# Kernel optimization log

Measured on AMD Instinct MI355X. Metric: run time of the kernel, lower is better.

The kernel has to match this reference:

```python
import jax, jax.numpy as jnp
import numpy as np

N, C_IN, H, W = 32, 16, 256, 256
C_OUT, K = 64, 3

def setup_inputs() -> dict:
    key = jax.random.key(0)
    kx, kw, kb = jax.random.split(key, 3)
    x = jax.random.normal(kx, (N, C_IN, H, W), dtype=jnp.float32)
    # PyTorch Conv2d default init: U(-b, b), b = 1/sqrt(fan_in)
    bound = 1.0 / np.sqrt(C_IN * K * K)
    conv_weight = jax.random.uniform(kw, (C_OUT, C_IN, K, K), minval=-bound, maxval=bound, dtype=jnp.float32)
    conv_bias = jax.random.uniform(kb, (C_OUT,), minval=-bound, maxval=bound, dtype=jnp.float32)
    return {"x": x, "conv_weight": conv_weight, "conv_bias": conv_bias}

def reference(x, conv_weight, conv_bias):
    # conv2d, stride=1, padding=0 (VALID), NCHW / OIHW
    y = jax.lax.conv_general_dilated(
        x, conv_weight,
        window_strides=(1, 1), padding="VALID",
        dimension_numbers=("NCHW", "OIHW", "NCHW"))
    y = y + conv_bias[None, :, None, None]
    # min over output channels (keepdim -> 1 channel), then double tanh
    y = jnp.min(y, axis=1, keepdims=True)  # [N,1,OH,OW]
    return jnp.tanh(jnp.tanh(y))
```

## Files before the change

kernel.cpp:

```cpp
#include <hip/hip_runtime.h>

typedef __bf16 bf16x8 __attribute__((ext_vector_type(8)));
typedef unsigned short us8 __attribute__((ext_vector_type(8)));
typedef unsigned short us2 __attribute__((ext_vector_type(2)));
typedef float f32x16 __attribute__((ext_vector_type(16)));

#define N_IMG 32
#define CI 16
#define HH 256
#define WW 256
#define CO 64
#define OHH 254
#define OWW 254

#define XS_W 258
#define SC 24
#define NSTRIP 24
#define WP_SHORTS (CO * 160)
#define WS_NEEDED ((size_t)WP_SHORTS * 2)

__device__ __forceinline__ unsigned short f2bf(float f) {
  union { float f; unsigned u; } v; v.f = f;
  return (unsigned short)((v.u + 0x7FFFu + ((v.u >> 16) & 1u)) >> 16);
}

#if defined(__has_builtin)
#if __has_builtin(__builtin_amdgcn_cvt_pk_bf16_f32)
#define HAVE_CVT_PK 1
#endif
#endif

__device__ __forceinline__ us2 cvt2(float a, float b) {
#ifdef HAVE_CVT_PK
  typedef __bf16 bf16x2 __attribute__((ext_vector_type(2)));
  bf16x2 r = __builtin_amdgcn_cvt_pk_bf16_f32(a, b);
  return __builtin_bit_cast(us2, r);
#else
  us2 r; r[0] = f2bf(a); r[1] = f2bf(b); return r;
#endif
}

__device__ __forceinline__ float fast_tanh(float x) {
  float cx = fminf(fmaxf(x, -15.f), 15.f);
  float e = __expf(2.f * cx);
  return (e - 1.f) / (e + 1.f);
}

__global__ void prep_w(const float* __restrict__ wg, const float* __restrict__ bg,
                       unsigned short* __restrict__ wp) {
  int idx = blockIdx.x * 256 + threadIdx.x;
  if (idx >= WP_SHORTS) return;
  int oc = idx / 160;
  int k = idx - oc * 160;
  int tap = k >> 4, ci = k & 15;
  float v;
  if (tap < 9)      v = wg[oc * 144 + ci * 9 + tap];
  else if (ci == 0) v = bg[oc];
  else              v = 0.f;
  wp[idx] = f2bf(v);
}

__global__ __launch_bounds__(256, 3)
void conv_fused(const float* __restrict__ xg, const unsigned short* __restrict__ wp,
                float* __restrict__ out) {
  __shared__ __align__(16) unsigned short xs[4 * XS_W * SC];
  const int t = threadIdx.x;
  const int n = blockIdx.x / NSTRIP;
  const int s = blockIdx.x - n * NSTRIP;
  const int oh0 = s * 10 + (s < 14 ? s : 14);
  const int nrows = (s < 14) ? 11 : 10;
  const int oh1 = oh0 + nrows;

  const float* srcT = xg + (size_t)n * (CI * HH * WW) + t;

  {
    float v[3][16];
#pragma unroll
    for (int r = 0; r < 3; ++r)
#pragma unroll
      for (int j = 0; j < 16; ++j)
        v[r][j] = srcT[((size_t)j * HH + (oh0 + r)) * WW];
#pragma unroll
    for (int r = 0; r < 3; ++r) {
      union { us8 v8[2]; us2 v2[8]; } pk;
#pragma unroll
      for (int j = 0; j < 8; ++j) pk.v2[j] = cvt2(v[r][2 * j], v[r][2 * j + 1]);
      const int slot = (oh0 + r) & 3;
      *(us8*)(xs + (slot * XS_W + t) * SC) = pk.v8[0];
      *(us8*)(xs + (slot * XS_W + t) * SC + 8) = pk.v8[1];
    }
  }
  if (t < 128) {
    const int slot = t >> 5, rem = t & 31;
    xs[(slot * XS_W + 256 + (rem >> 4)) * SC + (rem & 15)] = 0;
  }

  const int lane = t & 63, wave = t >> 6;
  const int lr = lane & 31, qh = lane >> 5;

  const unsigned short* wpl = wp + lr * 160 + qh * 8;
  bf16x8 afrag[2][10];
#pragma unroll
  for (int mt = 0; mt < 2; ++mt)
#pragma unroll
    for (int tap = 0; tap < 10; ++tap)
      afrag[mt][tap] =
          __builtin_bit_cast(bf16x8, *(const us8*)(wpl + mt * 32 * 160 + tap * 16));

  us8 onev = {};
  if (qh == 0) onev[0] = 0x3F80;
  const bf16x8 xone = __builtin_bit_cast(bf16x8, onev);

  const int pb = wave * 64;

  __syncthreads();

  for (int oh = oh0; oh < oh1; ++oh) {
    const bool do_stage = (oh + 1 < oh1);

    float v[16];
    if (do_stage) {
#pragma unroll
      for (int j = 0; j < 16; ++j)
        v[j] = srcT[((size_t)j * HH + (oh + 3)) * WW];
    }

    float vmin[2];
#pragma unroll
    for (int nt = 0; nt < 2; ++nt) {
      f32x16 acc0, acc1;
#pragma unroll
      for (int e = 0; e < 16; ++e) { acc0[e] = 0.f; acc1[e] = 0.f; }
#pragma unroll
      for (int tap = 0; tap < 9; ++tap) {
        const int kh = tap / 3, kw = tap - kh * 3;
        const int slot = (oh + kh) & 3;
        bf16x8 xf = __builtin_bit_cast(
            bf16x8,
            *(const us8*)(xs + (slot * XS_W + pb + nt * 32 + lr + kw) * SC + qh * 8));
        acc0 = __builtin_amdgcn_mfma_f32_32x32x16_bf16(afrag[0][tap], xf, acc0, 0, 0, 0);
        acc1 = __builtin_amdgcn_mfma_f32_32x32x16_bf16(afrag[1][tap], xf, acc1, 0, 0, 0);
      }
      acc0 = __builtin_amdgcn_mfma_f32_32x32x16_bf16(afrag[0][9], xone, acc0, 0, 0, 0);
      acc1 = __builtin_amdgcn_mfma_f32_32x32x16_bf16(afrag[1][9], xone, acc1, 0, 0, 0);

      float mv = acc0[0];
#pragma unroll
      for (int e = 1; e < 16; ++e) mv = fminf(mv, acc0[e]);
#pragma unroll
      for (int e = 0; e < 16; ++e) mv = fminf(mv, acc1[e]);
      mv = fminf(mv, __shfl_xor(mv, 32, 64));
      vmin[nt] = fast_tanh(fast_tanh(mv));
    }

    if (do_stage) {
      union { us8 v8[2]; us2 v2[8]; } pk;
#pragma unroll
      for (int j = 0; j < 8; ++j) pk.v2[j] = cvt2(v[2 * j], v[2 * j + 1]);
      const int slot = (oh + 3) & 3;
      *(us8*)(xs + (slot * XS_W + t) * SC) = pk.v8[0];
      *(us8*)(xs + (slot * XS_W + t) * SC + 8) = pk.v8[1];
    }

    const float res = (lane < 32) ? vmin[0] : vmin[1];
    const int ow = pb + lane;
    if (ow < OWW) out[((size_t)n * OHH + oh) * OWW + ow] = res;

    __syncthreads();
  }
}

#define XS_C 24
#define WS_K 168
__global__ __launch_bounds__(256, 2)
void conv_min_tanh(const float* __restrict__ xg, const float* __restrict__ wg,
                   const float* __restrict__ bg, float* __restrict__ out) {
  __shared__ __align__(16) unsigned short xs[3 * XS_W * XS_C];
  __shared__ __align__(16) unsigned short ws[CO * WS_K];
  const int t = threadIdx.x;
  const int n = blockIdx.x / OHH;
  const int oh = blockIdx.x % OHH;
#pragma unroll
  for (int i = 0; i < 36; ++i) {
    int f = i * 256 + t;
    int oc = f / 144;
    int r = f - oc * 144;
    int ci = r / 9;
    int tap = r - ci * 9;
    ws[oc * WS_K + tap * 16 + ci] = f2bf(wg[f]);
  }
  if (t < CO) ws[t * WS_K + 144] = f2bf(bg[t]);
  for (int i = t; i < CO * 15; i += 256) {
    int oc = i / 15;
    ws[oc * WS_K + 145 + (i - oc * 15)] = 0;
  }
  {
    const size_t base_n = (size_t)n * CI * HH * WW;
#pragma unroll
    for (int kh = 0; kh < 3; ++kh) {
#pragma unroll
      for (int half = 0; half < 2; ++half) {
        float v[8];
#pragma unroll
        for (int j = 0; j < 8; ++j) {
          int ci = half * 8 + j;
          v[j] = xg[base_n + ((size_t)ci * HH + (oh + kh)) * WW + t];
        }
        us8 pk;
#pragma unroll
        for (int j = 0; j < 8; ++j) pk[j] = f2bf(v[j]);
        *(us8*)(xs + (kh * XS_W + t) * XS_C + half * 8) = pk;
      }
    }
  }
  if (t < 96) {
    int kh = t >> 5;
    int rem = t & 31;
    int w = 256 + (rem >> 4);
    int ci = rem & 15;
    xs[(kh * XS_W + w) * XS_C + ci] = 0;
  }
  __syncthreads();
  const int lane = t & 63, wave = t >> 6;
  const int lr = lane & 31, qh = lane >> 5;
  bf16x8 afrag[2][10];
#pragma unroll
  for (int mt = 0; mt < 2; ++mt) {
    const unsigned short* wq = ws + (mt * 32 + lr) * WS_K + qh * 8;
#pragma unroll
    for (int tap = 0; tap < 10; ++tap)
      afrag[mt][tap] = __builtin_bit_cast(bf16x8, *(const us8*)(wq + tap * 16));
  }
  f32x16 acc[2][2];
#pragma unroll
  for (int a = 0; a < 2; ++a)
#pragma unroll
    for (int b = 0; b < 2; ++b)
#pragma unroll
      for (int e = 0; e < 16; ++e) acc[a][b][e] = 0.f;
  const unsigned short* xq = xs + (wave * 64 + lr) * XS_C + qh * 8;
#pragma unroll
  for (int tap = 0; tap < 9; ++tap) {
    const int kh = tap / 3, kw = tap - kh * 3;
#pragma unroll
    for (int nt = 0; nt < 2; ++nt) {
      bf16x8 xf = __builtin_bit_cast(
          bf16x8, *(const us8*)(xq + (kh * XS_W + nt * 32 + kw) * XS_C));
      acc[0][nt] = __builtin_amdgcn_mfma_f32_32x32x16_bf16(afrag[0][tap], xf,
                                                           acc[0][nt], 0, 0, 0);
      acc[1][nt] = __builtin_amdgcn_mfma_f32_32x32x16_bf16(afrag[1][tap], xf,
                                                           acc[1][nt], 0, 0, 0);
    }
  }
  {
    us8 one = {};
    if (qh == 0) one[0] = 0x3F80;
    bf16x8 xone = __builtin_bit_cast(bf16x8, one);
#pragma unroll
    for (int nt = 0; nt < 2; ++nt) {
      acc[0][nt] = __builtin_amdgcn_mfma_f32_32x32x16_bf16(afrag[0][9], xone,
                                                           acc[0][nt], 0, 0, 0);
      acc[1][nt] = __builtin_amdgcn_mfma_f32_32x32x16_bf16(afrag[1][9], xone,
                                                           acc[1][nt], 0, 0, 0);
    }
  }
  float vmin[2];
#pragma unroll
  for (int nt = 0; nt < 2; ++nt) {
    float v = acc[0][nt][0];
#pragma unroll
    for (int e = 1; e < 16; ++e) v = fminf(v, acc[0][nt][e]);
#pragma unroll
    for (int e = 0; e < 16; ++e) v = fminf(v, acc[1][nt][e]);
    v = fminf(v, __shfl_xor(v, 32, 64));
    vmin[nt] = fast_tanh(fast_tanh(v));
  }
  float res = (lane < 32) ? vmin[0] : vmin[1];
  int ow = wave * 64 + lane;
  if (ow < OWW) out[((size_t)n * OHH + oh) * OWW + ow] = res;
}

extern "C" void kernel_launch(void* const* d_in, const int* in_sizes, int n_in,
                              void* d_out, int out_size, void* d_ws, size_t ws_size,
                              hipStream_t stream) {
  const float* x = (const float*)d_in[0];
  const float* w = (const float*)d_in[1];
  const float* b = (const float*)d_in[2];
  float* out = (float*)d_out;
  if (ws_size >= WS_NEEDED) {
    unsigned short* wp = (unsigned short*)d_ws;
    prep_w<<<dim3((WP_SHORTS + 255) / 256), dim3(256), 0, stream>>>(w, b, wp);
    conv_fused<<<dim3(N_IMG * NSTRIP), dim3(256), 0, stream>>>(x, wp, out);
  } else {
    conv_min_tanh<<<dim3(N_IMG * OHH), dim3(256), 0, stream>>>(x, w, b, out);
  }
}
```

Measured before the change: 209.4 us.

## Give each wave a private LDS row window with halo to drop block barriers

Splits the shared row ring buffer into per-wave 66-column regions. Each wave stages its own 64 columns plus the 2-column halo, which it reloads redundantly from global memory. This removes both __syncthreads calls, the one after the prologue and the one per output row, so waves no longer wait on each other. The cost is extra halo global loads, scalar LDS stores and slightly more LDS. Correctness now depends on intra-wave ordering, with no explicit wave-level barrier between the LDS writes and reads.

```diff
diff --git a/kernel.cpp b/kernel.cpp
--- a/kernel.cpp
+++ b/kernel.cpp
@@ -13,8 +13,8 @@
 #define OHH 254
 #define OWW 254
 
-#define XS_W 258
 #define SC 24
+#define XW 66
 #define NSTRIP 24
 #define WP_SHORTS (CO * 160)
 #define WS_NEEDED ((size_t)WP_SHORTS * 2)
@@ -63,7 +63,7 @@
 __global__ __launch_bounds__(256, 3)
 void conv_fused(const float* __restrict__ xg, const unsigned short* __restrict__ wp,
                 float* __restrict__ out) {
-  __shared__ __align__(16) unsigned short xs[4 * XS_W * SC];
+  __shared__ __align__(16) unsigned short xs[4 * 4 * XW * SC];
   const int t = threadIdx.x;
   const int n = blockIdx.x / NSTRIP;
   const int s = blockIdx.x - n * NSTRIP;
@@ -71,32 +71,45 @@
   const int nrows = (s < 14) ? 11 : 10;
   const int oh1 = oh0 + nrows;
 
+  const int lane = t & 63, wave = t >> 6;
+  const int lr = lane & 31, qh = lane >> 5;
+  const int pb = wave * 64;
+
   const float* srcT = xg + (size_t)n * (CI * HH * WW) + t;
+  const bool do_halo = (lane < 32) && (wave < 3);
+  const float* srcH = xg + (size_t)n * (CI * HH * WW) +
+                      (size_t)(lane & 15) * HH * WW + (pb + 64 + (lane >> 4));
+  unsigned short* const wreg = xs + (size_t)wave * XW * SC;
+
+  if (wave == 3 && lane < 32) {
+#pragma unroll
+    for (int slot = 0; slot < 4; ++slot)
+      xs[((slot * 4 + 3) * XW + 64 + (lane >> 4)) * SC + (lane & 15)] = 0;
+  }
 
   {
     float v[3][16];
-#pragma unroll
-    for (int r = 0; r < 3; ++r)
+    float vh[3];
+#pragma unroll
+    for (int r = 0; r < 3; ++r) {
 #pragma unroll
       for (int j = 0; j < 16; ++j)
         v[r][j] = srcT[((size_t)j * HH + (oh0 + r)) * WW];
+      if (do_halo) vh[r] = srcH[(size_t)(oh0 + r) * WW];
+    }
 #pragma unroll
     for (int r = 0; r < 3; ++r) {
       union { us8 v8[2]; us2 v2[8]; } pk;
 #pragma unroll
       for (int j = 0; j < 8; ++j) pk.v2[j] = cvt2(v[r][2 * j], v[r][2 * j + 1]);
       const int slot = (oh0 + r) & 3;
-      *(us8*)(xs + (slot * XS_W + t) * SC) = pk.v8[0];
-      *(us8*)(xs + (slot * XS_W + t) * SC + 8) = pk.v8[1];
-    }
-  }
-  if (t < 128) {
-    const int slot = t >> 5, rem = t & 31;
-    xs[(slot * XS_W + 256 + (rem >> 4)) * SC + (rem & 15)] = 0;
-  }
-
-  const int lane = t & 63, wave = t >> 6;
-  const int lr = lane & 31, qh = lane >> 5;
+      unsigned short* cell = wreg + ((size_t)slot * 4 * XW + lane) * SC;
+      *(us8*)(cell) = pk.v8[0];
+      *(us8*)(cell + 8) = pk.v8[1];
+      if (do_halo)
+        wreg[(slot * 4 * XW + 64 + (lane >> 4)) * SC + (lane & 15)] = f2bf(vh[r]);
+    }
+  }
 
   const unsigned short* wpl = wp + lr * 160 + qh * 8;
   bf16x8 afrag[2][10];
@@ -111,18 +124,17 @@
   if (qh == 0) onev[0] = 0x3F80;
   const bf16x8 xone = __builtin_bit_cast(bf16x8, onev);
 
-  const int pb = wave * 64;
-
-  __syncthreads();
 
   for (int oh = oh0; oh < oh1; ++oh) {
     const bool do_stage = (oh + 1 < oh1);
 
     float v[16];
+    float vh;
     if (do_stage) {
 #pragma unroll
       for (int j = 0; j < 16; ++j)
         v[j] = srcT[((size_t)j * HH + (oh + 3)) * WW];
+      if (do_halo) vh = srcH[(size_t)(oh + 3) * WW];
     }
 
     float vmin[2];
@@ -136,8 +148,8 @@
         const int kh = tap / 3, kw = tap - kh * 3;
         const int slot = (oh + kh) & 3;
         bf16x8 xf = __builtin_bit_cast(
-            bf16x8,
-            *(const us8*)(xs + (slot * XS_W + pb + nt * 32 + lr + kw) * SC + qh * 8));
+            bf16x8, *(const us8*)(wreg + ((size_t)slot * 4 * XW + nt * 32 + lr + kw) *
+                                             SC + qh * 8));
         acc0 = __builtin_amdgcn_mfma_f32_32x32x16_bf16(afrag[0][tap], xf, acc0, 0, 0, 0);
         acc1 = __builtin_amdgcn_mfma_f32_32x32x16_bf16(afrag[1][tap], xf, acc1, 0, 0, 0);
       }
@@ -158,18 +170,20 @@
 #pragma unroll
       for (int j = 0; j < 8; ++j) pk.v2[j] = cvt2(v[2 * j], v[2 * j + 1]);
       const int slot = (oh + 3) & 3;
-      *(us8*)(xs + (slot * XS_W + t) * SC) = pk.v8[0];
-      *(us8*)(xs + (slot * XS_W + t) * SC + 8) = pk.v8[1];
+      unsigned short* cell = wreg + ((size_t)slot * 4 * XW + lane) * SC;
+      *(us8*)(cell) = pk.v8[0];
+      *(us8*)(cell + 8) = pk.v8[1];
+      if (do_halo)
+        wreg[(slot * 4 * XW + 64 + (lane >> 4)) * SC + (lane & 15)] = f2bf(vh);
     }
 
     const float res = (lane < 32) ? vmin[0] : vmin[1];
     const int ow = pb + lane;
     if (ow < OWW) out[((size_t)n * OHH + oh) * OWW + ow] = res;
-
-    __syncthreads();
-  }
-}
-
+  }
+}
+
+#define XS_W 258
 #define XS_C 24
 #define WS_K 168
 __global__ __launch_bounds__(256, 2)
```

Result: slower. 218.4 us (+4.3%).
